# Optimization experiments

Hardware: AMD Instinct MI355X
Metric: run time of the kernel (lower is better)

Reference implementation:

```python
import jax, jax.numpy as jnp
import numpy as np

NUM_CLASSES = 80
INPUT_SHAPE = (416.0, 416.0)
ANCHORS_MASK0 = np.array([6, 7, 8])
CONF_THRES = 0.5
NMS_THRES = 0.4
IMAGE_SHAPE = (416.0, 416.0)
MAX_DET = 100          # fixed-size padded NMS output (jit-compatible)
CLASS_OFFSET = 4096.0  # class-aware box offset == independent per-class NMS
NEG = jnp.float32(-1e9)


def setup_inputs() -> dict:
    key = jax.random.key(0)
    inputs_1 = jax.random.normal(key, (32, 255, 52, 52), dtype=jnp.float32)
    anchors = jnp.array([[10, 13], [16, 30], [33, 23], [30, 61], [62, 45],
                         [59, 119], [116, 90], [156, 198], [373, 326]], dtype=jnp.float32)
    return {"inputs_1": inputs_1, "anchors": anchors}


def _decode(inputs_1, anchors):
    B, C, H, W = inputs_1.shape
    A = len(ANCHORS_MASK0)
    attrs = C // A  # 5 + num_classes
    # [B, A, H, W, attrs]
    pred = inputs_1.reshape(B, A, attrs, H, W).transpose(0, 1, 3, 4, 2)
    xy = jax.nn.sigmoid(pred[..., 0:2])
    wh = pred[..., 2:4]
    conf = jax.nn.sigmoid(pred[..., 4])
    cls = jax.nn.sigmoid(pred[..., 5:])
    stride_h = INPUT_SHAPE[0] / H
    stride_w = INPUT_SHAPE[1] / W
    anc = anchors[ANCHORS_MASK0] / jnp.array([stride_w, stride_h], jnp.float32)  # [A,2]
    gx = jnp.arange(W, dtype=jnp.float32)
    gy = jnp.arange(H, dtype=jnp.float32)
    bx = xy[..., 0] + gx[None, None, None, :]
    by = xy[..., 1] + gy[None, None, :, None]
    bw = jnp.exp(wh[..., 0]) * anc[:, 0][None, :, None, None]
    bh = jnp.exp(wh[..., 1]) * anc[:, 1][None, :, None, None]
    boxes = jnp.stack([bx, by, bw, bh], -1) / jnp.array([W, H, W, H], jnp.float32)
    return jnp.concatenate([boxes.reshape(B, -1, 4),
                            conf.reshape(B, -1, 1),
                            cls.reshape(B, -1, NUM_CLASSES)], axis=-1)  # [B, A*H*W, 5+C]


def _iou(box, boxes):
    lt = jnp.maximum(box[:2], boxes[:, :2])
    rb = jnp.minimum(box[2:], boxes[:, 2:])
    wh = jnp.clip(rb - lt, 0.0)
    inter = wh[:, 0] * wh[:, 1]
    a1 = (box[2] - box[0]) * (box[3] - box[1])
    a2 = (boxes[:, 2] - boxes[:, 0]) * (boxes[:, 3] - boxes[:, 1])
    return inter / (a1 + a2 - inter + 1e-9)


def _nms(pred0):
    # pred0: [N, 5+C] (image 0, matching torch code which only processes prediction[0])
    cx, cy, w, h = pred0[:, 0], pred0[:, 1], pred0[:, 2], pred0[:, 3]
    corners = jnp.stack([cx - w / 2, cy - h / 2, cx + w / 2, cy + h / 2], -1)  # [N,4]
    class_conf = jnp.max(pred0[:, 5:], axis=1)
    class_pred = jnp.argmax(pred0[:, 5:], axis=1)
    score = pred0[:, 4] * class_conf  # obj_conf * class_conf, same score nms() receives
    valid = score >= CONF_THRES
    # offsetting boxes by class id makes a single NMS pass equivalent to the per-class loop
    obox = corners + (class_pred.astype(jnp.float32) * CLASS_OFFSET)[:, None]
    s0 = jnp.where(valid, score, NEG)

    def step(scores, _):
        i = jnp.argmax(scores)
        flag = scores[i] > NEG / 2
        iou = _iou(obox[i], obox)
        new_scores = jnp.where(iou > NMS_THRES, NEG, scores).at[i].set(NEG)
        return new_scores, (i, flag)

    _, (idxs, flags) = jax.lax.scan(step, s0, None, length=MAX_DET)
    det = jnp.concatenate([
        corners[idxs],                                  # x1,y1,x2,y2
        pred0[idxs, 4:5],                               # obj conf
        class_conf[idxs][:, None],                      # class conf
        class_pred[idxs].astype(jnp.float32)[:, None],  # class id
    ], axis=1)  # [MAX_DET, 7]
    # yolo_correct_boxes: xywh -> yx min/max scaled to image_shape
    box_xy = (det[:, 0:2] + det[:, 2:4]) / 2.0
    box_wh = det[:, 2:4] - det[:, 0:2]
    box_yx = box_xy[:, ::-1]
    box_hw = box_wh[:, ::-1]
    mins = box_yx - box_hw / 2.0
    maxes = box_yx + box_hw / 2.0
    scale = jnp.array([IMAGE_SHAPE[0], IMAGE_SHAPE[1], IMAGE_SHAPE[0], IMAGE_SHAPE[1]], jnp.float32)
    boxes_corr = jnp.concatenate([mins, maxes], axis=1) * scale
    det = jnp.concatenate([boxes_corr, det[:, 4:]], axis=1)
    return det * flags[:, None].astype(jnp.float32)  # zero-padded rows where no detection


def reference(inputs_1, anchors):
    out = _decode(inputs_1, anchors)   # [B, 3*H*W, 5+num_classes]
    det = _nms(out[0])                 # [MAX_DET, 7], padded fixed-size NMS result
    return (out, det)
```

## Files before the change

### kernel.cpp

```cpp
#include <hip/hip_runtime.h>
#include <math.h>

constexpr int An = 3;
constexpr int Wd = 52;
constexpr int HWn = 2704;
constexpr int ATT = 85;
constexpr int CH = 208;
constexpr int PITCH = 209;
constexpr int CHUNKS = 13;
constexpr int DEC_BLOCKS = 96 * CHUNKS;
constexpr int NC = An * HWn;
constexpr int NSORT = 8192;
constexpr int OUT_DEC = 32 * NC * ATT;
constexpr float NEGV = -1.0e9f;
constexpr int WS_SCORE_OFF = 65536;

__device__ __forceinline__ float sig_(float x) {
    return 1.0f / (1.0f + expf(-x));
}

__global__ void __launch_bounds__(128)
yolo_prep(const float* __restrict__ in, const float* __restrict__ anc,
          float* __restrict__ ws)
{
    const int n = blockIdx.x * 128 + threadIdx.x;
    if (n >= NC) return;
    const int a   = n / HWn;
    const int pos = n - a * HWn;
    const float* p = in + (size_t)a * 85 * HWn + pos;

    const float tx = p[0];
    const float ty = p[HWn];
    const float tw = p[2 * HWn];
    const float th = p[3 * HWn];
    const float tc = p[4 * HWn];

    float m = -3.0e38f; int cp = 0;
    #pragma unroll
    for (int j0 = 0; j0 < 80; j0 += 16) {
        float v[16];
        #pragma unroll
        for (int u = 0; u < 16; ++u) v[u] = p[(size_t)(5 + j0 + u) * HWn];
        #pragma unroll
        for (int u = 0; u < 16; ++u) {
            if (v[u] > m) { m = v[u]; cp = j0 + u; }
        }
    }

    const float cc    = sig_(m);
    const float conf  = sig_(tc);
    const float score = __fmul_rn(conf, cc);
    const float aw = anc[(6 + a) * 2 + 0] * 0.125f;
    const float ah = anc[(6 + a) * 2 + 1] * 0.125f;
    const float cx = (sig_(tx) + (float)(pos % Wd)) / 52.0f;
    const float cy = (sig_(ty) + (float)(pos / Wd)) / 52.0f;
    const float bw = expf(tw) * aw / 52.0f;
    const float bh = expf(th) * ah / 52.0f;
    const float hw = __fmul_rn(bw, 0.5f);
    const float hh = __fmul_rn(bh, 0.5f);
    float4* w4 = (float4*)ws;
    w4[2 * n + 0] = make_float4(__fsub_rn(cx, hw), __fsub_rn(cy, hh),
                                __fadd_rn(cx, hw), __fadd_rn(cy, hh));
    w4[2 * n + 1] = make_float4(conf, cc, (float)cp, 0.0f);
    ws[WS_SCORE_OFF + n] = score;
}

__global__ void __launch_bounds__(1024)
yolo_nms(const float* __restrict__ ws, float* __restrict__ out)
{
    __shared__ unsigned long long keys[NSORT];
    __shared__ float kept[100 * 4];
    __shared__ float detstage[100 * 7];
    __shared__ int   meta[2];
    const int tid = threadIdx.x;
    const unsigned lane = tid & 63;

    if (tid == 0) meta[0] = 0;
    __syncthreads();

    const float* wscore = ws + WS_SCORE_OFF;
    for (int k = 0; k < 8; ++k) {
        const int n = tid + k * 1024;
        const float s = (n < NC) ? wscore[n] : NEGV;
        const bool valid = (s >= 0.5f);
        const unsigned long long mask = __ballot(valid);
        if (mask != 0ULL) {
            const int leader = __ffsll((long long)mask) - 1;
            int base = 0;
            if ((int)lane == leader) base = atomicAdd(&meta[0], __popcll(mask));
            base = __shfl(base, leader);
            if (valid) {
                const int slot = base +
                    __popcll(mask & ((1ULL << lane) - 1ULL));
                keys[slot] =
                    ((unsigned long long)(0xFFFFFFFFu - __float_as_uint(s)) << 32)
                    | (unsigned)n;
            }
        }
    }
    __syncthreads();
    const int V = meta[0];
    int P2 = 1; while (P2 < V) P2 <<= 1;

    for (int i = V + tid; i < P2; i += 1024) keys[i] = ~0ULL;
    __syncthreads();

    for (int k = 2; k <= P2; k <<= 1) {
        for (int j = k >> 1; j > 0; j >>= 1) {
            for (int i = tid; i < P2; i += 1024) {
                const int l = i ^ j;
                if (l > i) {
                    const unsigned long long a = keys[i], b = keys[l];
                    const bool up = ((i & k) == 0);
                    if (up ? (b < a) : (a < b)) { keys[i] = b; keys[l] = a; }
                }
            }
            __syncthreads();
        }
    }

    if (tid < 64) {
        const float4* w4 = (const float4*)ws;
        float4* keptv = (float4*)kept;
        int nk = 0;

        float cx1 = 0, cy1 = 0, cx2 = 0, cy2 = 0, mconf = 0, mcc = 0, mcp = 0;
        bool act = (tid < V);
        if (act) {
            const int n = (int)(keys[tid] & 0xFFFFFFFFu);
            const float4 bx = w4[2 * n], mt = w4[2 * n + 1];
            cx1 = bx.x; cy1 = bx.y; cx2 = bx.z; cy2 = bx.w;
            mconf = mt.x; mcc = mt.y; mcp = mt.z;
        }

        for (int p0 = 0; p0 < V && nk < 100; p0 += 64) {
            float nx1 = 0, ny1 = 0, nx2 = 0, ny2 = 0, nco = 0, ncc = 0, ncp = 0;
            const bool actn = (p0 + 64 + tid) < V;
            if (actn) {
                const int n = (int)(keys[p0 + 64 + tid] & 0xFFFFFFFFu);
                const float4 bx = w4[2 * n], mt = w4[2 * n + 1];
                nx1 = bx.x; ny1 = bx.y; nx2 = bx.z; ny2 = bx.w;
                nco = mt.x; ncc = mt.y; ncp = mt.z;
            }

            const float off = __fmul_rn(mcp, 4096.0f);
            const float ox1 = __fadd_rn(cx1, off);
            const float oy1 = __fadd_rn(cy1, off);
            const float ox2 = __fadd_rn(cx2, off);
            const float oy2 = __fadd_rn(cy2, off);
            const float aC  = __fmul_rn(__fsub_rn(ox2, ox1), __fsub_rn(oy2, oy1));

            bool sup = !act;
            for (int t = 0; t < nk; ++t) {
                const float4 kb = keptv[t];
                const float ltx = fmaxf(kb.x, ox1), lty = fmaxf(kb.y, oy1);
                const float rbx = fminf(kb.z, ox2), rby = fminf(kb.w, oy2);
                const float iw = fmaxf(__fsub_rn(rbx, ltx), 0.0f);
                const float ih = fmaxf(__fsub_rn(rby, lty), 0.0f);
                const float inter = __fmul_rn(iw, ih);
                const float aK = __fmul_rn(__fsub_rn(kb.z, kb.x), __fsub_rn(kb.w, kb.y));
                const float den = __fadd_rn(__fsub_rn(__fadd_rn(aK, aC), inter), 1e-9f);
                if (inter / den > 0.4f) sup = true;
            }

            unsigned long long rem = __ballot(!sup);
            while (rem != 0ULL && nk < 100) {
                const int w = __ffsll((long long)rem) - 1;
                const float wx1 = __shfl(ox1, w), wy1 = __shfl(oy1, w);
                const float wx2 = __shfl(ox2, w), wy2 = __shfl(oy2, w);
                const float aW  = __shfl(aC, w);
                if (tid == w) {
                    keptv[nk] = make_float4(ox1, oy1, ox2, oy2);
                    float* dr = detstage + nk * 7;
                    const float xm  = __fmul_rn(__fadd_rn(cx1, cx2), 0.5f);
                    const float ym  = __fmul_rn(__fadd_rn(cy1, cy2), 0.5f);
                    const float hw2 = __fmul_rn(__fsub_rn(cx2, cx1), 0.5f);
                    const float hh2 = __fmul_rn(__fsub_rn(cy2, cy1), 0.5f);
                    dr[0] = __fmul_rn(__fsub_rn(ym, hh2), 416.0f);
                    dr[1] = __fmul_rn(__fsub_rn(xm, hw2), 416.0f);
                    dr[2] = __fmul_rn(__fadd_rn(ym, hh2), 416.0f);
                    dr[3] = __fmul_rn(__fadd_rn(xm, hw2), 416.0f);
                    dr[4] = mconf; dr[5] = mcc; dr[6] = mcp;
                }
                ++nk;
                if (!sup && tid > w) {
                    const float ltx = fmaxf(wx1, ox1), lty = fmaxf(wy1, oy1);
                    const float rbx = fminf(wx2, ox2), rby = fminf(wy2, oy2);
                    const float iw = fmaxf(__fsub_rn(rbx, ltx), 0.0f);
                    const float ih = fmaxf(__fsub_rn(rby, lty), 0.0f);
                    const float inter = __fmul_rn(iw, ih);
                    const float den = __fadd_rn(__fsub_rn(__fadd_rn(aW, aC), inter), 1e-9f);
                    if (inter / den > 0.4f) sup = true;
                }
                rem = __ballot(!sup && tid > w);
            }

            cx1 = nx1; cy1 = ny1; cx2 = nx2; cy2 = ny2;
            mconf = nco; mcc = ncc; mcp = ncp;
            act = actn;
        }
        if (tid == 0) meta[1] = nk;
    }
    __syncthreads();

    const int nk = meta[1];
    for (int i = tid; i < 100 * 7; i += 1024) {
        out[OUT_DEC + i] = (i < nk * 7) ? detstage[i] : 0.0f;
    }
}

__global__ void __launch_bounds__(1024)
yolo_decode(const float* __restrict__ in, const float* __restrict__ anc,
            float* __restrict__ out)
{
    extern __shared__ float smem[];
    const int tid = threadIdx.x;
    const int bi    = (int)blockIdx.x;
    const int chunk = bi % CHUNKS;
    const int ba    = bi / CHUNKS;
    const int a     = ba % An;
    const float anc_w = anc[(6 + a) * 2 + 0] * 0.125f;
    const float anc_h = anc[(6 + a) * 2 + 1] * 0.125f;
    const int pos0  = chunk * CH;
    const float* src = in + (size_t)ba * 85 * HWn + pos0;

    for (int i = tid; i < ATT * CH; i += 1024) {
        const int attr = i / CH;
        const int p    = i - attr * CH;
        const int pos  = pos0 + p;
        const float x  = src[(size_t)attr * HWn + p];
        float v;
        if (attr >= 4)      v = sig_(x);
        else if (attr == 0) v = (sig_(x) + (float)(pos % Wd)) / 52.0f;
        else if (attr == 1) v = (sig_(x) + (float)(pos / Wd)) / 52.0f;
        else if (attr == 2) v = expf(x) * anc_w / 52.0f;
        else                v = expf(x) * anc_h / 52.0f;
        smem[attr * PITCH + p] = v;
    }
    __syncthreads();

    float* dst = out + ((size_t)ba * HWn + pos0) * ATT;
    for (int f = tid; f < CH * ATT; f += 1024) {
        const int p    = f / ATT;
        const int attr = f - p * ATT;
        dst[f] = smem[attr * PITCH + p];
    }
}

extern "C" void kernel_launch(void* const* d_in, const int* in_sizes, int n_in,
                              void* d_out, int out_size, void* d_ws, size_t ws_size,
                              hipStream_t stream) {
    const float* in  = (const float*)d_in[0];
    const float* anc = (const float*)d_in[1];
    float* out = (float*)d_out;
    float* ws  = (float*)d_ws;

    hipLaunchKernelGGL(yolo_prep, dim3((NC + 127) / 128), dim3(128), 0, stream,
                       in, anc, ws);
    hipLaunchKernelGGL(yolo_nms, dim3(1), dim3(1024), 0, stream, ws, out);
    const size_t shmem = (size_t)(ATT * PITCH) * sizeof(float);
    hipLaunchKernelGGL(yolo_decode, dim3(DEC_BLOCKS), dim3(1024), shmem, stream,
                       in, anc, out);
}
```

Before: 273.7 us.

## Fuse NMS and decode into one launch and parallelize NMS across block

Merges the single-block NMS kernel and the decode kernel into one launch. Block 0 runs NMS while the remaining blocks decode, so the long serial NMS overlaps the bandwidth-bound decode instead of running before it. NMS now uses all 1024 threads per candidate batch, finding winners through per-wave ballots and an LDS min-reduction with block barriers, instead of one wave scanning 64 at a time. The bitonic sort enumerates only compare pairs. Decode gets float4 loads and stores with a pitch padded to a multiple of four. In exchange, every block reserves the larger dynamic LDS, and NMS pays two block barriers per kept box.

```diff
diff --git a/kernel.cpp b/kernel.cpp
--- a/kernel.cpp
+++ b/kernel.cpp
@@ -6,14 +6,14 @@
 constexpr int HWn = 2704;
 constexpr int ATT = 85;
 constexpr int CH = 208;
-constexpr int PITCH = 209;
+constexpr int PITCH = 212;
 constexpr int CHUNKS = 13;
 constexpr int DEC_BLOCKS = 96 * CHUNKS;
 constexpr int NC = An * HWn;
-constexpr int NSORT = 8192;
 constexpr int OUT_DEC = 32 * NC * ATT;
 constexpr float NEGV = -1.0e9f;
 constexpr int WS_SCORE_OFF = 65536;
+constexpr size_t DEC_LDS = (size_t)ATT * PITCH * sizeof(float);
 
 __device__ __forceinline__ float sig_(float x) {
     return 1.0f / (1.0f + expf(-x));
@@ -66,14 +66,68 @@
 }
 
 __global__ void __launch_bounds__(1024)
-yolo_nms(const float* __restrict__ ws, float* __restrict__ out)
+yolo_fused(const float* __restrict__ in, const float* __restrict__ anc,
+           float* __restrict__ out, const float* __restrict__ ws)
 {
-    __shared__ unsigned long long keys[NSORT];
-    __shared__ float kept[100 * 4];
-    __shared__ float detstage[100 * 7];
-    __shared__ int   meta[2];
+    extern __shared__ float dynsm[];
     const int tid = threadIdx.x;
-    const unsigned lane = tid & 63;
+
+    if (blockIdx.x != 0) {
+        const int bi    = (int)blockIdx.x - 1;
+        const int chunk = bi % CHUNKS;
+        const int ba    = bi / CHUNKS;
+        const int a     = ba % An;
+        const float anc_w = anc[(6 + a) * 2 + 0] * 0.125f;
+        const float anc_h = anc[(6 + a) * 2 + 1] * 0.125f;
+        const int pos0  = chunk * CH;
+        const float* src = in + (size_t)ba * 85 * HWn + pos0;
+        const float gy0 = (float)(chunk * 4);
+
+        for (int i = tid; i < ATT * 52; i += 1024) {
+            const int attr = i / 52;
+            const int q    = i - attr * 52;
+            const float4 x = *(const float4*)(src + (size_t)attr * HWn + 4 * q);
+            const float xs[4] = {x.x, x.y, x.z, x.w};
+            float v[4];
+            #pragma unroll
+            for (int u = 0; u < 4; ++u) {
+                const int pp = 4 * q + u;
+                float val;
+                if (attr >= 4)      val = sig_(xs[u]);
+                else if (attr == 0) val = (sig_(xs[u]) + (float)(pp % 52)) / 52.0f;
+                else if (attr == 1) val = (sig_(xs[u]) + (gy0 + (float)(pp / 52))) / 52.0f;
+                else if (attr == 2) val = expf(xs[u]) * anc_w / 52.0f;
+                else                val = expf(xs[u]) * anc_h / 52.0f;
+                v[u] = val;
+            }
+            *(float4*)(dynsm + attr * PITCH + 4 * q) = make_float4(v[0], v[1], v[2], v[3]);
+        }
+        __syncthreads();
+
+        float* dst = out + ((size_t)ba * HWn + pos0) * ATT;
+        for (int j = tid; j < ATT * 52; j += 1024) {
+            const int f0 = 4 * j;
+            float v[4];
+            #pragma unroll
+            for (int u = 0; u < 4; ++u) {
+                const int g  = f0 + u;
+                const int p  = g / 85;
+                const int at = g - 85 * p;
+                v[u] = dynsm[at * PITCH + p];
+            }
+            *(float4*)(dst + f0) = make_float4(v[0], v[1], v[2], v[3]);
+        }
+        return;
+    }
+
+    unsigned long long* keys = (unsigned long long*)dynsm;
+    float* kept     = dynsm + 16384;
+    float* detstage = kept + 400;
+    float* winslot  = detstage + 700;
+    int*   wavemin  = (int*)(winslot + 8);
+    int*   meta     = wavemin + 16;
+    const int lane = tid & 63;
+    const int wv   = tid >> 6;
 
     if (tid == 0) meta[0] = 0;
     __syncthreads();
@@ -87,11 +141,10 @@
         if (mask != 0ULL) {
             const int leader = __ffsll((long long)mask) - 1;
             int base = 0;
-            if ((int)lane == leader) base = atomicAdd(&meta[0], __popcll(mask));
+            if (lane == leader) base = atomicAdd(&meta[0], __popcll(mask));
             base = __shfl(base, leader);
             if (valid) {
-                const int slot = base +
-                    __popcll(mask & ((1ULL << lane) - 1ULL));
+                const int slot = base + __popcll(mask & ((1ULL << lane) - 1ULL));
                 keys[slot] =
                     ((unsigned long long)(0xFFFFFFFFu - __float_as_uint(s)) << 32)
                     | (unsigned)n;
@@ -101,57 +154,41 @@
     __syncthreads();
     const int V = meta[0];
     int P2 = 1; while (P2 < V) P2 <<= 1;
-
     for (int i = V + tid; i < P2; i += 1024) keys[i] = ~0ULL;
     __syncthreads();
 
     for (int k = 2; k <= P2; k <<= 1) {
         for (int j = k >> 1; j > 0; j >>= 1) {
-            for (int i = tid; i < P2; i += 1024) {
-                const int l = i ^ j;
-                if (l > i) {
-                    const unsigned long long a = keys[i], b = keys[l];
-                    const bool up = ((i & k) == 0);
-                    if (up ? (b < a) : (a < b)) { keys[i] = b; keys[l] = a; }
-                }
+            for (int idx = tid; idx < (P2 >> 1); idx += 1024) {
+                const int i = ((idx & ~(j - 1)) << 1) | (idx & (j - 1));
+                const int l = i | j;
+                const unsigned long long a = keys[i], b = keys[l];
+                const bool up = ((i & k) == 0);
+                if (up ? (b < a) : (a < b)) { keys[i] = b; keys[l] = a; }
             }
             __syncthreads();
         }
     }
 
-    if (tid < 64) {
-        const float4* w4 = (const float4*)ws;
-        float4* keptv = (float4*)kept;
-        int nk = 0;
-
-        float cx1 = 0, cy1 = 0, cx2 = 0, cy2 = 0, mconf = 0, mcc = 0, mcp = 0;
-        bool act = (tid < V);
+    const float4* w4 = (const float4*)ws;
+    float4* keptv = (float4*)kept;
+    int nk = 0;
+    for (int sb = 0; sb * 1024 < V && nk < 100; ++sb) {
+        const int cidx = sb * 1024 + tid;
+        const bool act = (cidx < V);
+        float rx1 = 0, ry1 = 0, rx2 = 0, ry2 = 0, mconf = 0, mcc = 0, mcp = 0;
+        float ox1 = 0, oy1 = 0, ox2 = 0, oy2 = 0, aC = 0;
+        bool alive = act;
         if (act) {
-            const int n = (int)(keys[tid] & 0xFFFFFFFFu);
+            const int n = (int)(keys[cidx] & 0xFFFFFFFFu);
             const float4 bx = w4[2 * n], mt = w4[2 * n + 1];
-            cx1 = bx.x; cy1 = bx.y; cx2 = bx.z; cy2 = bx.w;
+            rx1 = bx.x; ry1 = bx.y; rx2 = bx.z; ry2 = bx.w;
             mconf = mt.x; mcc = mt.y; mcp = mt.z;
-        }
-
-        for (int p0 = 0; p0 < V && nk < 100; p0 += 64) {
-            float nx1 = 0, ny1 = 0, nx2 = 0, ny2 = 0, nco = 0, ncc = 0, ncp = 0;
-            const bool actn = (p0 + 64 + tid) < V;
-            if (actn) {
-                const int n = (int)(keys[p0 + 64 + tid] & 0xFFFFFFFFu);
-                const float4 bx = w4[2 * n], mt = w4[2 * n + 1];
-                nx1 = bx.x; ny1 = bx.y; nx2 = bx.z; ny2 = bx.w;
-                nco = mt.x; ncc = mt.y; ncp = mt.z;
-            }
-
             const float off = __fmul_rn(mcp, 4096.0f);
-            const float ox1 = __fadd_rn(cx1, off);
-            const float oy1 = __fadd_rn(cy1, off);
-            const float ox2 = __fadd_rn(cx2, off);
-            const float oy2 = __fadd_rn(cy2, off);
-            const float aC  = __fmul_rn(__fsub_rn(ox2, ox1), __fsub_rn(oy2, oy1));
-
-            bool sup = !act;
-            for (int t = 0; t < nk; ++t) {
+            ox1 = __fadd_rn(rx1, off); oy1 = __fadd_rn(ry1, off);
+            ox2 = __fadd_rn(rx2, off); oy2 = __fadd_rn(ry2, off);
+            aC  = __fmul_rn(__fsub_rn(ox2, ox1), __fsub_rn(oy2, oy1));
+            for (int t = 0; t < nk && alive; ++t) {
                 const float4 kb = keptv[t];
                 const float ltx = fmaxf(kb.x, ox1), lty = fmaxf(kb.y, oy1);
                 const float rbx = fminf(kb.z, ox2), rby = fminf(kb.w, oy2);
@@ -160,90 +197,60 @@
                 const float inter = __fmul_rn(iw, ih);
                 const float aK = __fmul_rn(__fsub_rn(kb.z, kb.x), __fsub_rn(kb.w, kb.y));
                 const float den = __fadd_rn(__fsub_rn(__fadd_rn(aK, aC), inter), 1e-9f);
-                if (inter / den > 0.4f) sup = true;
-            }
-
-            unsigned long long rem = __ballot(!sup);
-            while (rem != 0ULL && nk < 100) {
-                const int w = __ffsll((long long)rem) - 1;
-                const float wx1 = __shfl(ox1, w), wy1 = __shfl(oy1, w);
-                const float wx2 = __shfl(ox2, w), wy2 = __shfl(oy2, w);
-                const float aW  = __shfl(aC, w);
-                if (tid == w) {
-                    keptv[nk] = make_float4(ox1, oy1, ox2, oy2);
-                    float* dr = detstage + nk * 7;
-                    const float xm  = __fmul_rn(__fadd_rn(cx1, cx2), 0.5f);
-                    const float ym  = __fmul_rn(__fadd_rn(cy1, cy2), 0.5f);
-                    const float hw2 = __fmul_rn(__fsub_rn(cx2, cx1), 0.5f);
-                    const float hh2 = __fmul_rn(__fsub_rn(cy2, cy1), 0.5f);
-                    dr[0] = __fmul_rn(__fsub_rn(ym, hh2), 416.0f);
-                    dr[1] = __fmul_rn(__fsub_rn(xm, hw2), 416.0f);
-                    dr[2] = __fmul_rn(__fadd_rn(ym, hh2), 416.0f);
-                    dr[3] = __fmul_rn(__fadd_rn(xm, hw2), 416.0f);
-                    dr[4] = mconf; dr[5] = mcc; dr[6] = mcp;
-                }
-                ++nk;
-                if (!sup && tid > w) {
-                    const float ltx = fmaxf(wx1, ox1), lty = fmaxf(wy1, oy1);
-                    const float rbx = fminf(wx2, ox2), rby = fminf(wy2, oy2);
-                    const float iw = fmaxf(__fsub_rn(rbx, ltx), 0.0f);
-                    const float ih = fmaxf(__fsub_rn(rby, lty), 0.0f);
-                    const float inter = __fmul_rn(iw, ih);
-                    const float den = __fadd_rn(__fsub_rn(__fadd_rn(aW, aC), inter), 1e-9f);
-                    if (inter / den > 0.4f) sup = true;
-                }
-                rem = __ballot(!sup && tid > w);
-            }
-
-            cx1 = nx1; cy1 = ny1; cx2 = nx2; cy2 = ny2;
-            mconf = nco; mcc = ncc; mcp = ncp;
-            act = actn;
-        }
-        if (tid == 0) meta[1] = nk;
-    }
-    __syncthreads();
-
-    const int nk = meta[1];
+                if (inter / den > 0.4f) alive = false;
+            }
+        }
+        if (tid == 0) {
+            winslot[0] = 4e9f; winslot[1] = 4e9f; winslot[2] = 4e9f; winslot[3] = 4e9f;
+            winslot[4] = 0.0f;
+        }
+        __syncthreads();
+
+        while (true) {
+            if (alive) {
+                const float wx1 = winslot[0], wy1 = winslot[1];
+                const float wx2 = winslot[2], wy2 = winslot[3], aW = winslot[4];
+                const float ltx = fmaxf(wx1, ox1), lty = fmaxf(wy1, oy1);
+                const float rbx = fminf(wx2, ox2), rby = fminf(wy2, oy2);
+                const float iw = fmaxf(__fsub_rn(rbx, ltx), 0.0f);
+                const float ih = fmaxf(__fsub_rn(rby, lty), 0.0f);
+                const float inter = __fmul_rn(iw, ih);
+                const float den = __fadd_rn(__fsub_rn(__fadd_rn(aW, aC), inter), 1e-9f);
+                if (inter / den > 0.4f) alive = false;
+            }
+            const unsigned long long m = __ballot(alive);
+            if (lane == 0)
+                wavemin[wv] = m ? (wv * 64 + (__ffsll((long long)m) - 1)) : 0x7FFFFFFF;
+            __syncthreads();
+            int win = 0x7FFFFFFF;
+            #pragma unroll
+            for (int w = 0; w < 16; ++w) win = min(win, wavemin[w]);
+            if (win == 0x7FFFFFFF) break;
+            if (tid == win) {
+                winslot[0] = ox1; winslot[1] = oy1; winslot[2] = ox2; winslot[3] = oy2;
+                winslot[4] = aC;
+                keptv[nk] = make_float4(ox1, oy1, ox2, oy2);
+                float* dr = detstage + nk * 7;
+                const float xm  = __fmul_rn(__fadd_rn(rx1, rx2), 0.5f);
+                const float ym  = __fmul_rn(__fadd_rn(ry1, ry2), 0.5f);
+                const float hw2 = __fmul_rn(__fsub_rn(rx2, rx1), 0.5f);
+                const float hh2 = __fmul_rn(__fsub_rn(ry2, ry1), 0.5f);
+                dr[0] = __fmul_rn(__fsub_rn(ym, hh2), 416.0f);
+                dr[1] = __fmul_rn(__fsub_rn(xm, hw2), 416.0f);
+                dr[2] = __fmul_rn(__fadd_rn(ym, hh2), 416.0f);
+                dr[3] = __fmul_rn(__fadd_rn(xm, hw2), 416.0f);
+                dr[4] = mconf; dr[5] = mcc; dr[6] = mcp;
+                alive = false;
+            }
+            __syncthreads();
+            ++nk;
+            if (nk == 100) break;
+        }
+    }
+    __syncthreads();
+
     for (int i = tid; i < 100 * 7; i += 1024) {
         out[OUT_DEC + i] = (i < nk * 7) ? detstage[i] : 0.0f;
-    }
-}
-
-__global__ void __launch_bounds__(1024)
-yolo_decode(const float* __restrict__ in, const float* __restrict__ anc,
-            float* __restrict__ out)
-{
-    extern __shared__ float smem[];
-    const int tid = threadIdx.x;
-    const int bi    = (int)blockIdx.x;
-    const int chunk = bi % CHUNKS;
-    const int ba    = bi / CHUNKS;
-    const int a     = ba % An;
-    const float anc_w = anc[(6 + a) * 2 + 0] * 0.125f;
-    const float anc_h = anc[(6 + a) * 2 + 1] * 0.125f;
-    const int pos0  = chunk * CH;
-    const float* src = in + (size_t)ba * 85 * HWn + pos0;
-
-    for (int i = tid; i < ATT * CH; i += 1024) {
-        const int attr = i / CH;
-        const int p    = i - attr * CH;
-        const int pos  = pos0 + p;
-        const float x  = src[(size_t)attr * HWn + p];
-        float v;
-        if (attr >= 4)      v = sig_(x);
-        else if (attr == 0) v = (sig_(x) + (float)(pos % Wd)) / 52.0f;
-        else if (attr == 1) v = (sig_(x) + (float)(pos / Wd)) / 52.0f;
-        else if (attr == 2) v = expf(x) * anc_w / 52.0f;
-        else                v = expf(x) * anc_h / 52.0f;
-        smem[attr * PITCH + p] = v;
-    }
-    __syncthreads();
-
-    float* dst = out + ((size_t)ba * HWn + pos0) * ATT;
-    for (int f = tid; f < CH * ATT; f += 1024) {
-        const int p    = f / ATT;
-        const int attr = f - p * ATT;
-        dst[f] = smem[attr * PITCH + p];
     }
 }
 
@@ -257,8 +264,6 @@
 
     hipLaunchKernelGGL(yolo_prep, dim3((NC + 127) / 128), dim3(128), 0, stream,
                        in, anc, ws);
-    hipLaunchKernelGGL(yolo_nms, dim3(1), dim3(1024), 0, stream, ws, out);
-    const size_t shmem = (size_t)(ATT * PITCH) * sizeof(float);
-    hipLaunchKernelGGL(yolo_decode, dim3(DEC_BLOCKS), dim3(1024), shmem, stream,
-                       in, anc, out);
-}
+    hipLaunchKernelGGL(yolo_fused, dim3(DEC_BLOCKS + 1), dim3(1024), DEC_LDS,
+                       stream, in, anc, out, ws);
+}
```

Result: faster. 235.6 us (-14.0%).
